# Performance work log

Hardware: AMD Instinct MI355X
Metric: run time of the kernel (lower is better)

Reference implementation:

```python
import jax, jax.numpy as jnp
import numpy as np

D_MODEL = 2048
NUM_HEADS = 16
D_K = D_MODEL // NUM_HEADS


def _xavier(key, shape):
    # xavier_uniform_ for a (fan_in, fan_out) matrix
    limit = np.sqrt(6.0 / (shape[0] + shape[1]))
    return jax.random.uniform(key, shape, dtype=jnp.float32, minval=-limit, maxval=limit)


def setup_inputs() -> dict:
    key = jax.random.key(0)
    kx, kq, kk, kv, ko = jax.random.split(key, 5)
    x = jax.random.normal(kx, (4, 2048, D_MODEL), dtype=jnp.float32)
    return {
        "x": x,
        "w_q": _xavier(kq, (D_MODEL, D_MODEL)),
        "w_k": _xavier(kk, (D_MODEL, D_MODEL)),
        "w_v": _xavier(kv, (D_MODEL, D_MODEL)),
        "w_o": _xavier(ko, (D_MODEL, D_MODEL)),
    }


def _split_heads(t):
    b, s, _ = t.shape
    return t.reshape(b, s, NUM_HEADS, D_K).transpose(0, 2, 1, 3)  # [b,h,s,dk]


def reference(x, w_q, w_k, w_v, w_o):
    q = _split_heads(x @ w_q)
    k = _split_heads(x @ w_k)
    v = _split_heads(x @ w_v)
    scale = 1.0 / np.sqrt(D_K).astype(np.float32)
    scores = jnp.einsum("bhqd,bhkd->bhqk", q, k) * scale
    attn = jax.nn.softmax(scores, axis=-1)
    out = jnp.einsum("bhqk,bhkd->bhqd", attn, v)  # [b,h,s,dk]
    b, h, s, dk = out.shape
    out = out.transpose(0, 2, 1, 3).reshape(b, s, h * dk)
    return out @ w_o
```

## Files before the change

### kernel.cpp

```cpp
#include <hip/hip_runtime.h>
#include <hip/hip_bf16.h>

typedef __attribute__((ext_vector_type(8))) __bf16 bf16x8;
typedef __attribute__((ext_vector_type(4))) __bf16 bf16x4;
typedef __attribute__((ext_vector_type(4))) float f32x4;
typedef __attribute__((ext_vector_type(16))) float f32x16;
typedef __attribute__((ext_vector_type(8))) unsigned short u16x8;
typedef unsigned short u16;

#define DEVINL static __device__ __forceinline__

namespace {
constexpr int kB = 4;
constexpr int kS = 2048;
constexpr int kDM = 2048;
constexpr int kH = 16;
constexpr int kDK = 128;
constexpr int kM = kB * kS;
constexpr int kNQKV = 3 * kDM;
constexpr float kE2 = 0.08838834764831845f * 1.44269504088896f;
}

DEVINL u16 f2bf(float f) {
  __hip_bfloat16 h = __float2bfloat16(f);
  return __builtin_bit_cast(u16, h);
}

#if __has_builtin(__builtin_amdgcn_exp2f)
DEVINL float exp2_fast(float x) { return __builtin_amdgcn_exp2f(x); }
#else
DEVINL float exp2_fast(float x) { return exp2f(x); }
#endif

#define GLOAD16(gp, lp) \
  __builtin_amdgcn_global_load_lds((const __attribute__((address_space(1))) void*)(gp), \
                                   (__attribute__((address_space(3))) void*)(lp), 16, 0, 0)

DEVINL bf16x8 lds_frag(const u16* p) { return *reinterpret_cast<const bf16x8*>(p); }

DEVINL f32x4 MFMA16x16(bf16x8 a, bf16x8 b, f32x4 c) {
  return __builtin_amdgcn_mfma_f32_16x16x32_bf16(a, b, c, 0, 0, 0);
}

struct TrueT { static constexpr bool value = true; };
struct FalseT { static constexpr bool value = false; };

__global__ __launch_bounds__(256) void cast_x_kernel(const float* __restrict__ x,
                                                     u16* __restrict__ o, int n4) {
  int i = blockIdx.x * 256 + threadIdx.x;
  if (i >= n4) return;
  float4 v = reinterpret_cast<const float4*>(x)[i];
  ushort4 r;
  r.x = f2bf(v.x); r.y = f2bf(v.y); r.z = f2bf(v.z); r.w = f2bf(v.w);
  reinterpret_cast<ushort4*>(o)[i] = r;
}

__global__ __launch_bounds__(256) void transpose_w_kernel(const float* __restrict__ w0,
    const float* __restrict__ w1, const float* __restrict__ w2, const float* __restrict__ w3,
    u16* __restrict__ wtcat, u16* __restrict__ wot) {
  const float* src = (blockIdx.z == 0) ? w0 : (blockIdx.z == 1) ? w1
                    : (blockIdx.z == 2) ? w2 : w3;
  u16* dst = (blockIdx.z < 3) ? (wtcat + (size_t)blockIdx.z * kDM * kDM) : wot;
  __shared__ float tile[32][33];
  int n0 = blockIdx.x * 32, k0 = blockIdx.y * 32;
  int tx = threadIdx.x, ty = threadIdx.y;
#pragma unroll
  for (int i = 0; i < 4; ++i)
    tile[ty + i * 8][tx] = src[(size_t)(k0 + ty + i * 8) * kDM + n0 + tx];
  __syncthreads();
#pragma unroll
  for (int i = 0; i < 4; ++i)
    dst[(size_t)(n0 + ty + i * 8) * kDM + k0 + tx] = f2bf(tile[tx][ty + i * 8]);
}

__global__ __launch_bounds__(256) void transpose_v_kernel(const u16* __restrict__ qkv,
                                                          u16* __restrict__ vt) {
  int bh = blockIdx.z, b = bh >> 4, h = bh & 15;
  int s0 = blockIdx.x * 32, d0 = blockIdx.y * 32;
  __shared__ u16 tile[32][33];
  int tx = threadIdx.x, ty = threadIdx.y;
#pragma unroll
  for (int i = 0; i < 4; ++i)
    tile[ty + i * 8][tx] =
        qkv[(size_t)(b * kS + s0 + ty + i * 8) * kNQKV + 2 * kDM + h * kDK + d0 + tx];
  __syncthreads();
#pragma unroll
  for (int i = 0; i < 4; ++i)
    vt[(size_t)(bh * kDK + d0 + ty + i * 8) * kS + s0 + tx] = tile[tx][ty + i * 8];
}

DEVINL void cstore(float* p, float v) { *p = v; }
DEVINL void cstore(u16* p, float v) { *p = f2bf(v); }

#define PH_OPEN()                                      \
  __builtin_amdgcn_sched_barrier(0);                   \
  __builtin_amdgcn_s_barrier();                        \
  asm volatile("s_waitcnt lgkmcnt(0)" ::: "memory");   \
  __builtin_amdgcn_sched_barrier(0);                   \
  __builtin_amdgcn_s_setprio(1)

#define PH_CLOSE()                                     \
  __builtin_amdgcn_s_setprio(0);                       \
  __builtin_amdgcn_sched_barrier(0);                   \
  __builtin_amdgcn_s_barrier()

#define PH_CLOSE_G4()                                  \
  __builtin_amdgcn_s_setprio(0);                       \
  __builtin_amdgcn_sched_barrier(0);                   \
  asm volatile("s_waitcnt vmcnt(4)" ::: "memory");     \
  __builtin_amdgcn_sched_barrier(0);                   \
  __builtin_amdgcn_s_barrier()

#define PH_CLOSE_G0()                                  \
  __builtin_amdgcn_s_setprio(0);                       \
  __builtin_amdgcn_sched_barrier(0);                   \
  asm volatile("s_waitcnt vmcnt(0)" ::: "memory");     \
  __builtin_amdgcn_sched_barrier(0);                   \
  __builtin_amdgcn_s_barrier()

#define RD_A(SB, MQ, DST)                                             \
  do {                                                                \
    _Pragma("unroll") for (int mf = 0; mf < 4; ++mf) {                \
      const u16* p_ = (SB) + (awrow + (MQ) * 64 + mf * 16) * 64;      \
      DST[mf * 2 + 0] = lds_frag(p_ + g0);                            \
      DST[mf * 2 + 1] = lds_frag(p_ + g1);                            \
    }                                                                 \
  } while (0)

#define RD_BH(SB, NH)                                                 \
  do {                                                                \
    _Pragma("unroll") for (int nf = 0; nf < 2; ++nf) {                \
      const u16* p_ = (SB) + (bwrow + (NH) * 32 + nf * 16) * 64;      \
      b[(NH) * 4 + nf * 2 + 0] = lds_frag(p_ + g0);                   \
      b[(NH) * 4 + nf * 2 + 1] = lds_frag(p_ + g1);                   \
    }                                                                 \
  } while (0)

#define MMQ(MQ, NH, AF)                                               \
  do {                                                                \
    _Pragma("unroll") for (int mf = 0; mf < 4; ++mf)                  \
      _Pragma("unroll") for (int nf = 0; nf < 2; ++nf) {              \
        f32x4 t_ = acc[(MQ) * 4 + mf][(NH) * 2 + nf];                 \
        t_ = MFMA16x16(AF[mf * 2 + 0], b[(NH) * 4 + nf * 2 + 0], t_); \
        t_ = MFMA16x16(AF[mf * 2 + 1], b[(NH) * 4 + nf * 2 + 1], t_); \
        acc[(MQ) * 4 + mf][(NH) * 2 + nf] = t_;                       \
      }                                                               \
  } while (0)

#define STG_A(buf, R0, kt) \
  GLOAD16(baseA + (size_t)(R0) * lda + (size_t)(kt) * 64, ldsA + (buf) * 16384 + (R0) * 64)
#define STG_B(buf, R0, kt) \
  GLOAD16(baseB + (size_t)(R0) * ldb + (size_t)(kt) * 64, ldsB + (buf) * 16384 + (R0) * 64)

template <typename CT>
__global__ __launch_bounds__(512, 2) void gemm256_kernel(const u16* __restrict__ A,
    const u16* __restrict__ Bt, CT* __restrict__ C, int K, int lda, int ldb, int ldc) {
  __shared__ __align__(16) u16 sA[2][16384];
  __shared__ __align__(16) u16 sB[2][16384];
  const int tid = threadIdx.x;
  const int lane = tid & 63, wid = tid >> 6;
  const int r15 = lane & 15, hi = lane >> 4;
  const int wm = wid >> 2, wn = wid & 3;

  const int gx = gridDim.x, nwg = gx * gridDim.y;
  const int orig = blockIdx.y * gx + blockIdx.x;
  const int wg = (orig & 7) * (nwg >> 3) + (orig >> 3);
  const int n0 = (wg % gx) * 256;
  const int m0 = (wg / gx) * 256;

  const int NT = K >> 6;
  const int NITER = NT >> 1;

  const int rc = tid >> 3;
  const int cg = (tid & 7) ^ (rc & 7);
  const u16* baseA = A + (size_t)(m0 + rc) * lda + cg * 8;
  const u16* baseB = Bt + (size_t)(n0 + rc) * ldb + cg * 8;
  u16* ldsA = &sA[0][0] + rc * 64 + (tid & 7) * 8;
  u16* ldsB = &sB[0][0] + rc * 64 + (tid & 7) * 8;

  const int sw = r15 & 7;
  const int g0 = (hi ^ sw) * 8;
  const int g1 = ((4 + hi) ^ sw) * 8;
  const int awrow = wm * 128 + r15;
  const int bwrow = wn * 64 + r15;
  const u16* sA0 = &sA[0][0]; const u16* sA1 = &sA[1][0];
  const u16* sB0 = &sB[0][0]; const u16* sB1 = &sB[1][0];

  f32x4 acc[8][4] = {};
  bf16x8 aE[8], aO[8], b[8];

  STG_A(0, 0, 0); STG_A(0, 64, 0); STG_A(0, 128, 0); STG_A(0, 192, 0);
  STG_B(0, 0, 0); STG_B(0, 64, 0); STG_B(0, 128, 0); STG_B(0, 192, 0);
  STG_A(1, 0, 1); STG_A(1, 128, 1);
  STG_B(1, 0, 1); STG_B(1, 64, 1); STG_B(1, 128, 1); STG_B(1, 192, 1);
  asm volatile("s_waitcnt vmcnt(6)" ::: "memory");
  __builtin_amdgcn_sched_barrier(0);
  __builtin_amdgcn_s_barrier();
  RD_A(sA0, 0, aE); RD_BH(sB0, 0);

  int kb = 0;
  auto iter = [&](auto lastc) {
    constexpr bool L = decltype(lastc)::value;
    const int kO = kb + 1, k2 = kb + 2, k3 = kb + 3;
    STG_A(1, 64, kO); STG_A(1, 192, kO);
    PH_OPEN();
    RD_BH(sB0, 1);
    MMQ(0, 0, aE);
    PH_CLOSE();
    if constexpr (!L) { STG_A(0, 0, k2); STG_A(0, 128, k2); }
    PH_OPEN();
    RD_A(sA0, 1, aO);
    MMQ(0, 1, aE);
    PH_CLOSE();
    if constexpr (!L) { STG_B(0, 0, k2); STG_B(0, 64, k2); }
    PH_OPEN();
    MMQ(1, 0, aO);
    if constexpr (L) { PH_CLOSE_G0(); } else { PH_CLOSE_G4(); }
    if constexpr (!L) { STG_B(0, 128, k2); STG_B(0, 192, k2); }
    PH_OPEN();
    RD_A(sA1, 0, aE); RD_BH(sB1, 0);
    MMQ(1, 1, aO);
    PH_CLOSE();
    if constexpr (!L) { STG_A(0, 64, k2); STG_A(0, 192, k2); }
    PH_OPEN();
    RD_BH(sB1, 1);
    MMQ(0, 0, aE);
    PH_CLOSE();
    if constexpr (!L) { STG_A(1, 0, k3); STG_A(1, 128, k3); }
    PH_OPEN();
    RD_A(sA1, 1, aO);
    MMQ(0, 1, aE);
    PH_CLOSE();
    if constexpr (!L) { STG_B(1, 0, k3); STG_B(1, 64, k3); }
    PH_OPEN();
    MMQ(1, 0, aO);
    if constexpr (L) { PH_CLOSE_G0(); } else { PH_CLOSE_G4(); }
    if constexpr (!L) { STG_B(1, 128, k3); STG_B(1, 192, k3); }
    PH_OPEN();
    if constexpr (!L) { RD_A(sA0, 0, aE); RD_BH(sB0, 0); }
    MMQ(1, 1, aO);
    PH_CLOSE();
    kb += 2;
  };
  for (int i = 0; i < NITER - 1; ++i) iter(FalseT{});
  iter(TrueT{});

  const size_t crow0 = (size_t)(m0 + wm * 128 + hi * 4);
  const int col0 = n0 + wn * 64 + r15;
#pragma unroll
  for (int im = 0; im < 8; ++im)
#pragma unroll
    for (int in = 0; in < 4; ++in)
#pragma unroll
      for (int r = 0; r < 4; ++r)
        cstore(&C[(crow0 + im * 16 + r) * ldc + col0 + in * 16], acc[im][in][r]);
}

__global__ __launch_bounds__(256, 2) void attn_kernel(const u16* __restrict__ qkv,
    const u16* __restrict__ vt, u16* __restrict__ attn_out) {
  __shared__ __align__(16) u16 lds[2][16384];
  const int tid = threadIdx.x;
  const int lane = tid & 63, wid = tid >> 6;
  const int l31 = lane & 31, hi5 = lane >> 5;
  const int q0 = blockIdx.x * 128, h = blockIdx.y, b = blockIdx.z;
  const int bh = b * kH + h;

  const int krow = tid >> 4, kg = tid & 15;
  const u16* kp = qkv + (size_t)(b * kS + krow) * kNQKV + kDM + h * kDK
                  + (size_t)((kg ^ (krow & 7)) * 8);
  const int vrow = tid >> 3, vg = tid & 7;
  const u16* vp = vt + (size_t)(bh * kDK + vrow) * kS + (size_t)((vg ^ (vrow & 7)) * 8);

  auto stage_kv = [&](u16* dst) {
#pragma unroll
    for (int i = 0; i < 4; ++i)
      GLOAD16(kp + (size_t)i * 16 * kNQKV, dst + (tid + 256 * i) * 8);
#pragma unroll
    for (int i = 0; i < 4; ++i)
      GLOAD16(vp + (size_t)i * 32 * kS, dst + 8192 + (tid + 256 * i) * 8);
    kp += (size_t)64 * kNQKV;
    vp += 64;
  };

#pragma unroll
  for (int i = 0; i < 8; ++i) {
    int row = (tid >> 4) + 16 * i;
    GLOAD16(qkv + (size_t)(b * kS + q0 + row) * kNQKV + h * kDK
                + (size_t)(((tid & 15) ^ (row & 7)) * 8),
            (u16*)lds[1] + (tid + 256 * i) * 8);
  }
  stage_kv(lds[0]);
  __syncthreads();

  bf16x8 qf[8];
  {
    const int qrow = wid * 32 + l31;
    const u16* qb = (const u16*)lds[1];
#pragma unroll
    for (int ds = 0; ds < 8; ++ds) {
      int slot = (ds * 2 + hi5) ^ (qrow & 7);
      qf[ds] = lds_frag(&qb[qrow * 128 + slot * 8]);
    }
  }
  __syncthreads();

  f32x16 o[4] = {};
  float mi = -1e30f, li = 0.f;
  int cur = 0;

  for (int t = 0; t < kS / 64; ++t) {
    if (t < kS / 64 - 1) stage_kv(lds[cur ^ 1]);

    const u16* Kb = (const u16*)lds[cur];
    const u16* Vb = Kb + 8192;

    f32x16 s0 = {}, s1 = {};
    const int kr = l31;
#pragma unroll
    for (int ds = 0; ds < 8; ++ds) {
      int slot = ((ds * 2 + hi5) ^ (kr & 7)) * 8;
      bf16x8 k0 = lds_frag(&Kb[kr * 128 + slot]);
      bf16x8 k1 = lds_frag(&Kb[(32 + kr) * 128 + slot]);
      s0 = __builtin_amdgcn_mfma_f32_32x32x16_bf16(k0, qf[ds], s0, 0, 0, 0);
      s1 = __builtin_amdgcn_mfma_f32_32x32x16_bf16(k1, qf[ds], s1, 0, 0, 0);
    }

    float mx = s0[0];
#pragma unroll
    for (int r = 1; r < 16; ++r) mx = fmaxf(mx, s0[r]);
#pragma unroll
    for (int r = 0; r < 16; ++r) mx = fmaxf(mx, s1[r]);
    mx = fmaxf(mx, __shfl_xor(mx, 32));
    float mc = mx * kE2;
    if (__any(mc > mi + 8.0f)) {
      float mn = fmaxf(mi, mc);
      float corr = exp2_fast(mi - mn);
      mi = mn;
      li *= corr;
#pragma unroll
      for (int r = 0; r < 16; ++r) {
        float c = __shfl(corr, (r & 3) + 8 * (r >> 2) + 4 * hi5);
        o[0][r] *= c; o[1][r] *= c; o[2][r] *= c; o[3][r] *= c;
      }
    }
    float p0[16], p1[16];
    float rs = 0.f;
#pragma unroll
    for (int r = 0; r < 16; ++r) { p0[r] = exp2_fast(s0[r] * kE2 - mi); rs += p0[r]; }
#pragma unroll
    for (int r = 0; r < 16; ++r) { p1[r] = exp2_fast(s1[r] * kE2 - mi); rs += p1[r]; }
    rs += __shfl_xor(rs, 32);
    li += rs;

    u16x8 pw0, pw1, pw2, pw3;
#pragma unroll
    for (int r = 0; r < 8; ++r) {
      pw0[r] = f2bf(p0[r]);
      pw1[r] = f2bf(p0[r + 8]);
      pw2[r] = f2bf(p1[r]);
      pw3[r] = f2bf(p1[r + 8]);
    }
    bf16x8 pa[4] = {__builtin_bit_cast(bf16x8, pw0), __builtin_bit_cast(bf16x8, pw1),
                    __builtin_bit_cast(bf16x8, pw2), __builtin_bit_cast(bf16x8, pw3)};

#pragma unroll
    for (int dt = 0; dt < 4; ++dt) {
      const int row = dt * 32 + l31;
      const int rs8 = row & 7;
#pragma unroll
      for (int ks = 0; ks < 4; ++ks) {
        bf16x4 vlo = *reinterpret_cast<const bf16x4*>(
            &Vb[row * 64 + ((ks * 2) ^ rs8) * 8 + hi5 * 4]);
        bf16x4 vhi = *reinterpret_cast<const bf16x4*>(
            &Vb[row * 64 + ((ks * 2 + 1) ^ rs8) * 8 + hi5 * 4]);
        bf16x8 bv = __builtin_shufflevector(vlo, vhi, 0, 1, 2, 3, 4, 5, 6, 7);
        o[dt] = __builtin_amdgcn_mfma_f32_32x32x16_bf16(pa[ks], bv, o[dt], 0, 0, 0);
      }
    }

    __syncthreads();
    cur ^= 1;
  }

  float rli = 1.0f / li;
  const size_t obase = (size_t)(b * kS + q0 + wid * 32) * kDM + h * kDK + l31;
#pragma unroll
  for (int r = 0; r < 16; ++r) {
    int ql = (r & 3) + 8 * (r >> 2) + 4 * hi5;
    float w = __shfl(rli, ql);
#pragma unroll
    for (int dt = 0; dt < 4; ++dt)
      attn_out[obase + (size_t)ql * kDM + dt * 32] = f2bf(o[dt][r] * w);
  }
}

extern "C" void kernel_launch(void* const* d_in, const int* in_sizes, int n_in,
                              void* d_out, int out_size, void* d_ws, size_t ws_size,
                              hipStream_t stream) {
  (void)in_sizes; (void)n_in; (void)out_size; (void)ws_size;
  const float* x  = (const float*)d_in[0];
  const float* wq = (const float*)d_in[1];
  const float* wk = (const float*)d_in[2];
  const float* wv = (const float*)d_in[3];
  const float* wo = (const float*)d_in[4];

  char* p = (char*)d_ws;
  u16* xb   = (u16*)p; p += (size_t)kM * kDM * 2;
  u16* wtc  = (u16*)p; p += (size_t)kNQKV * kDM * 2;
  u16* wot  = (u16*)p; p += (size_t)kDM * kDM * 2;
  u16* qkvb = (u16*)p; p += (size_t)kM * kNQKV * 2;
  u16* vtb  = (u16*)p; p += (size_t)kB * kH * kDK * kS * 2;
  u16* aob  = xb;

  int n4 = kM * kDM / 4;
  cast_x_kernel<<<(n4 + 255) / 256, 256, 0, stream>>>(x, xb, n4);
  transpose_w_kernel<<<dim3(kDM / 32, kDM / 32, 4), dim3(32, 8), 0, stream>>>(
      wq, wk, wv, wo, wtc, wot);
  gemm256_kernel<u16><<<dim3(kNQKV / 256, kM / 256), 512, 0, stream>>>(
      xb, wtc, qkvb, kDM, kDM, kDM, kNQKV);
  transpose_v_kernel<<<dim3(kS / 32, kDK / 32, kB * kH), dim3(32, 8), 0, stream>>>(
      qkvb, vtb);
  attn_kernel<<<dim3(kS / 128, kH, kB), 256, 0, stream>>>(qkvb, vtb, aob);
  gemm256_kernel<float><<<dim3(kDM / 256, kM / 256), 512, 0, stream>>>(
      aob, wot, (float*)d_out, kDM, kDM, kDM, kDM);
}
```

Baseline: 460.3 us.

## Fuse V transpose into QKV GEMM epilogue and widen attention V reads

The QKV projection GEMM now writes the V columns straight into the transposed per-head layout from its epilogue, so the separate transpose_v kernel and its extra read/write pass over V are gone. The output rows inside each 16-row fragment are permuted (hswap) so each lane stores four contiguous bf16 values, and the attention kernel's V fragment loads become single 8-element LDS reads to match. This saves a kernel launch and a full round-trip of V through memory. The cost is scattered, strided 8-byte stores in the GEMM epilogue and a correctness dependence on the permuted layout agreeing with the attention kernel's K-order.

```diff
diff --git a/kernel.cpp b/kernel.cpp
--- a/kernel.cpp
+++ b/kernel.cpp
@@ -2,7 +2,6 @@
 #include <hip/hip_bf16.h>
 
 typedef __attribute__((ext_vector_type(8))) __bf16 bf16x8;
-typedef __attribute__((ext_vector_type(4))) __bf16 bf16x4;
 typedef __attribute__((ext_vector_type(4))) float f32x4;
 typedef __attribute__((ext_vector_type(16))) float f32x16;
 typedef __attribute__((ext_vector_type(8))) unsigned short u16x8;
@@ -71,22 +70,6 @@
 #pragma unroll
   for (int i = 0; i < 4; ++i)
     dst[(size_t)(n0 + ty + i * 8) * kDM + k0 + tx] = f2bf(tile[tx][ty + i * 8]);
-}
-
-__global__ __launch_bounds__(256) void transpose_v_kernel(const u16* __restrict__ qkv,
-                                                          u16* __restrict__ vt) {
-  int bh = blockIdx.z, b = bh >> 4, h = bh & 15;
-  int s0 = blockIdx.x * 32, d0 = blockIdx.y * 32;
-  __shared__ u16 tile[32][33];
-  int tx = threadIdx.x, ty = threadIdx.y;
-#pragma unroll
-  for (int i = 0; i < 4; ++i)
-    tile[ty + i * 8][tx] =
-        qkv[(size_t)(b * kS + s0 + ty + i * 8) * kNQKV + 2 * kDM + h * kDK + d0 + tx];
-  __syncthreads();
-#pragma unroll
-  for (int i = 0; i < 4; ++i)
-    vt[(size_t)(bh * kDK + d0 + ty + i * 8) * kS + s0 + tx] = tile[tx][ty + i * 8];
 }
 
 DEVINL void cstore(float* p, float v) { *p = v; }
@@ -152,9 +135,10 @@
 #define STG_B(buf, R0, kt) \
   GLOAD16(baseB + (size_t)(R0) * ldb + (size_t)(kt) * 64, ldsB + (buf) * 16384 + (R0) * 64)
 
-template <typename CT>
+template <typename CT, bool WRITEV>
 __global__ __launch_bounds__(512, 2) void gemm256_kernel(const u16* __restrict__ A,
-    const u16* __restrict__ Bt, CT* __restrict__ C, int K, int lda, int ldb, int ldc) {
+    const u16* __restrict__ Bt, CT* __restrict__ C, u16* __restrict__ Vt,
+    int K, int lda, int ldb, int ldc) {
   __shared__ __align__(16) u16 sA[2][16384];
   __shared__ __align__(16) u16 sB[2][16384];
   const int tid = threadIdx.x;
@@ -245,6 +229,28 @@
   for (int i = 0; i < NITER - 1; ++i) iter(FalseT{});
   iter(TrueT{});
 
+  if constexpr (WRITEV) {
+    if (n0 >= 2 * kDM) {
+      const int hswap = ((hi & 1) << 1) | (hi >> 1);
+#pragma unroll
+      for (int im = 0; im < 8; ++im) {
+        const int m_base = m0 + wm * 128 + im * 16;
+        const int bq = m_base >> 11;
+        const int sp = (m_base & (kS - 1)) + hswap * 4;
+#pragma unroll
+        for (int in = 0; in < 4; ++in) {
+          const int c = n0 - 2 * kDM + wn * 64 + in * 16 + r15;
+          const int hh = c >> 7, dd = c & 127;
+          u16* dst = Vt + ((size_t)((bq * kH + hh) * kDK + dd)) * kS + sp;
+          ushort4 pk;
+          pk.x = f2bf(acc[im][in][0]); pk.y = f2bf(acc[im][in][1]);
+          pk.z = f2bf(acc[im][in][2]); pk.w = f2bf(acc[im][in][3]);
+          *reinterpret_cast<ushort4*>(dst) = pk;
+        }
+      }
+      return;
+    }
+  }
   const size_t crow0 = (size_t)(m0 + wm * 128 + hi * 4);
   const int col0 = n0 + wn * 64 + r15;
 #pragma unroll
@@ -369,11 +375,7 @@
       const int rs8 = row & 7;
 #pragma unroll
       for (int ks = 0; ks < 4; ++ks) {
-        bf16x4 vlo = *reinterpret_cast<const bf16x4*>(
-            &Vb[row * 64 + ((ks * 2) ^ rs8) * 8 + hi5 * 4]);
-        bf16x4 vhi = *reinterpret_cast<const bf16x4*>(
-            &Vb[row * 64 + ((ks * 2 + 1) ^ rs8) * 8 + hi5 * 4]);
-        bf16x8 bv = __builtin_shufflevector(vlo, vhi, 0, 1, 2, 3, 4, 5, 6, 7);
+        bf16x8 bv = lds_frag(&Vb[row * 64 + ((ks * 2 + hi5) ^ rs8) * 8]);
         o[dt] = __builtin_amdgcn_mfma_f32_32x32x16_bf16(pa[ks], bv, o[dt], 0, 0, 0);
       }
     }
@@ -416,11 +418,9 @@
   cast_x_kernel<<<(n4 + 255) / 256, 256, 0, stream>>>(x, xb, n4);
   transpose_w_kernel<<<dim3(kDM / 32, kDM / 32, 4), dim3(32, 8), 0, stream>>>(
       wq, wk, wv, wo, wtc, wot);
-  gemm256_kernel<u16><<<dim3(kNQKV / 256, kM / 256), 512, 0, stream>>>(
-      xb, wtc, qkvb, kDM, kDM, kDM, kNQKV);
-  transpose_v_kernel<<<dim3(kS / 32, kDK / 32, kB * kH), dim3(32, 8), 0, stream>>>(
-      qkvb, vtb);
+  gemm256_kernel<u16, true><<<dim3(kNQKV / 256, kM / 256), 512, 0, stream>>>(
+      xb, wtc, qkvb, vtb, kDM, kDM, kDM, kNQKV);
   attn_kernel<<<dim3(kS / 128, kH, kB), 256, 0, stream>>>(qkvb, vtb, aob);
-  gemm256_kernel<float><<<dim3(kDM / 256, kM / 256), 512, 0, stream>>>(
-      aob, wot, (float*)d_out, kDM, kDM, kDM, kDM);
-}
+  gemm256_kernel<float, false><<<dim3(kDM / 256, kM / 256), 512, 0, stream>>>(
+      aob, wot, (float*)d_out, nullptr, kDM, kDM, kDM, kDM);
+}
```

Result: faster. 440.4 us (-4.3%).
